# Kernel optimization log

Hardware: AMD Instinct MI355X
Metric: run time of the kernel (lower is better)

The kernel has to match this reference:

```python
import jax, jax.numpy as jnp
import numpy as np

BN_EPS = 1e-5


def setup_inputs() -> dict:
    key = jax.random.key(0)
    k0, k1, k2 = jax.random.split(key, 3)
    N, K, Cin, Cout = 300000, 27, 32, 64
    data = jax.random.normal(k0, (N, Cin), dtype=jnp.float32)
    # Octree neighbor table: index of the neighbor node for each of the 27
    # stencil offsets (-1 would mean empty; here all indices are valid).
    neigh = jax.random.randint(k1, (N, K), 0, N, dtype=jnp.int64)
    # Conv weight, one [Cin, Cout] matrix per stencil offset.
    weight = jax.random.normal(k2, (K, Cin, Cout), dtype=jnp.float32) * (1.0 / np.sqrt(K * Cin))
    gamma = jnp.ones((Cout,), dtype=jnp.float32)
    beta = jnp.zeros((Cout,), dtype=jnp.float32)
    return {"data": data, "neigh": neigh, "weight": weight, "gamma": gamma, "beta": beta}


def reference(data, neigh, weight, gamma, beta):
    # --- OctreeConv: gather neighbors (im2col over sparse octree) + matmul ---
    mask = neigh >= 0                                   # [N, K] valid-neighbor mask
    idx = jnp.clip(neigh, 0)
    gathered = jnp.where(mask[..., None], data[idx], 0.0)  # [N, K, Cin]
    out = jnp.einsum('nkc,kco->no', gathered, weight)       # [N, Cout]
    # --- BatchNorm1d (training mode: batch statistics over nodes) ---
    mean = jnp.mean(out, axis=0)
    var = jnp.var(out, axis=0)
    out = (out - mean) * jax.lax.rsqrt(var + BN_EPS) * gamma + beta
    # --- ReLU ---
    return jax.nn.relu(out)
```

## Files before the change

kernel.cpp:

```cpp
#include <hip/hip_runtime.h>

#define N_NODES   300000
#define K_STENCIL 27
#define CIN       32
#define COUT      64
#define BN_EPS    1e-5f

#define WS_STATS_OFF 0
#define WS_AB_OFF    32768
#define WS_CNT_OFF   33280
#define WS_WT_OFF    33792
#define N_SPLITS     64

typedef short bf16x8 __attribute__((ext_vector_type(8)));
typedef float f32x4  __attribute__((ext_vector_type(4)));

__device__ __forceinline__ short f2bf_rne(float f) {
    unsigned u = __builtin_bit_cast(unsigned, f);
    u += 0x7fffu + ((u >> 16) & 1u);
    return (short)(u >> 16);
}

__global__ __launch_bounds__(256) void prep(const float* __restrict__ w,
                                            unsigned short* __restrict__ wT,
                                            float* __restrict__ stats,
                                            unsigned int* __restrict__ cnt) {
    int t = blockIdx.x * blockDim.x + threadIdx.x;
    if (t < N_SPLITS * 128) stats[t] = 0.f;
    if (t == 0) *cnt = 0u;
    if (t < K_STENCIL * COUT * CIN) {
        int c = t & (CIN - 1);
        int o = (t >> 5) & (COUT - 1);
        int k = t >> 11;
        wT[t] = (unsigned short)f2bf_rne(w[(k * CIN + c) * COUT + o]);
    }
}

__global__ __launch_bounds__(256, 2) void conv_mfma(
        const float* __restrict__ data, const int* __restrict__ neigh,
        const unsigned short* __restrict__ wT, float* __restrict__ out) {
    const int wave  = threadIdx.x >> 6;
    const int lane  = threadIdx.x & 63;
    const int row16 = lane & 15;
    const int quad  = lane >> 4;

    bf16x8 ia, tb;
    #pragma unroll
    for (int j = 0; j < 8; ++j) {
        int k = quad * 8 + j;
        ia[j] = (k == row16) ? (short)0x3F80 : (short)0;
        tb[j] = f2bf_rne((float)(k * 16 + row16));
    }
    f32x4 pacc = {0.f, 0.f, 0.f, 0.f};
    pacc = __builtin_amdgcn_mfma_f32_16x16x32_bf16(ia, tb, pacc, 0, 0, 0);
    int mrow[4], ncol[4];
    #pragma unroll
    for (int r = 0; r < 4; ++r) {
        int iv = (int)(pacc[r] + 0.5f);
        mrow[r] = (iv >> 4) & 15;
        ncol[r] = iv & 15;
    }

    const int node   = blockIdx.x * 64 + wave * 16 + row16;
    const bool valid = (node < N_NODES);
    const int nclamp = valid ? node : 0;

    f32x4 acc[4] = {f32x4{0,0,0,0}, f32x4{0,0,0,0}, f32x4{0,0,0,0}, f32x4{0,0,0,0}};
    const int* nrow = neigh + nclamp * K_STENCIL;

    #pragma unroll
    for (int g = 0; g < 3; ++g) {
        int kid[9];
        #pragma unroll
        for (int j = 0; j < 9; ++j) kid[j] = nrow[g * 9 + j];

        f32x4 lo[9], hi[9];
        #pragma unroll
        for (int j = 0; j < 9; ++j) {
            int idx = kid[j];
            if (valid && idx >= 0) {
                const f32x4* drow = (const f32x4*)(data + (size_t)idx * CIN + quad * 8);
                lo[j] = drow[0];
                hi[j] = drow[1];
            } else {
                lo[j] = f32x4{0, 0, 0, 0};
                hi[j] = f32x4{0, 0, 0, 0};
            }
        }

        #pragma unroll
        for (int j = 0; j < 9; ++j) {
            bf16x8 afrag;
            #pragma unroll
            for (int t = 0; t < 4; ++t) {
                afrag[t]     = f2bf_rne(lo[j][t]);
                afrag[t + 4] = f2bf_rne(hi[j][t]);
            }
            const unsigned short* wk = wT + (g * 9 + j) * (COUT * CIN) + row16 * CIN + quad * 8;
            #pragma unroll
            for (int ct = 0; ct < 4; ++ct) {
                bf16x8 bfrag = *(const bf16x8*)(wk + ct * 16 * CIN);
                acc[ct] = __builtin_amdgcn_mfma_f32_16x16x32_bf16(afrag, bfrag, acc[ct], 0, 0, 0);
            }
        }
    }

    const int tilebase = blockIdx.x * 64 + wave * 16;
    #pragma unroll
    for (int ct = 0; ct < 4; ++ct) {
        #pragma unroll
        for (int r = 0; r < 4; ++r) {
            int n_out = tilebase + mrow[r];
            if (n_out < N_NODES)
                out[(size_t)n_out * COUT + ct * 16 + ncol[r]] = acc[ct][r];
        }
    }
}

__global__ __launch_bounds__(256) void stats_fin(const float* __restrict__ out,
                                                 float* __restrict__ stats,
                                                 unsigned int* __restrict__ cnt,
                                                 const float* __restrict__ gamma,
                                                 const float* __restrict__ beta,
                                                 float* __restrict__ ab) {
    __shared__ float lsum[COUT];
    __shared__ float lsq[COUT];
    __shared__ int lastFlag;
    if (threadIdx.x < COUT) { lsum[threadIdx.x] = 0.f; lsq[threadIdx.x] = 0.f; }
    __syncthreads();

    const int j = threadIdx.x & 15;
    int row = blockIdx.x * 16 + (threadIdx.x >> 4);
    const int rstride = gridDim.x * 16;
    float s0=0,s1=0,s2=0,s3=0,q0=0,q1=0,q2=0,q3=0;
    for (; row < N_NODES; row += rstride) {
        f32x4 v = ((const f32x4*)out)[row * 16 + j];
        s0 += v[0]; q0 += v[0]*v[0];
        s1 += v[1]; q1 += v[1]*v[1];
        s2 += v[2]; q2 += v[2]*v[2];
        s3 += v[3]; q3 += v[3]*v[3];
    }
    atomicAdd(&lsum[j*4+0], s0); atomicAdd(&lsq[j*4+0], q0);
    atomicAdd(&lsum[j*4+1], s1); atomicAdd(&lsq[j*4+1], q1);
    atomicAdd(&lsum[j*4+2], s2); atomicAdd(&lsq[j*4+2], q2);
    atomicAdd(&lsum[j*4+3], s3); atomicAdd(&lsq[j*4+3], q3);
    __syncthreads();

    if (threadIdx.x < 128) {
        int split = blockIdx.x & (N_SPLITS - 1);
        float v = (threadIdx.x < 64) ? lsum[threadIdx.x] : lsq[threadIdx.x - 64];
        atomicAdd(&stats[split * 128 + threadIdx.x], v);
    }
    __syncthreads();

    if (threadIdx.x == 0) {
        __threadfence();
        unsigned old = atomicAdd(cnt, 1u);
        lastFlag = (old == gridDim.x - 1) ? 1 : 0;
    }
    __syncthreads();

    if (lastFlag && threadIdx.x < COUT) {
        int o = threadIdx.x;
        float s = 0.f, q = 0.f;
        for (int sp = 0; sp < N_SPLITS; ++sp) {
            s += __hip_atomic_load(&stats[sp * 128 + o],
                                   __ATOMIC_RELAXED, __HIP_MEMORY_SCOPE_AGENT);
            q += __hip_atomic_load(&stats[sp * 128 + 64 + o],
                                   __ATOMIC_RELAXED, __HIP_MEMORY_SCOPE_AGENT);
        }
        float inv_n = 1.0f / (float)N_NODES;
        float mean = s * inv_n;
        float var  = q * inv_n - mean * mean;
        float a = gamma[o] * rsqrtf(var + BN_EPS);
        float b = beta[o] - mean * a;
        ab[o] = a;
        ab[64 + o] = b;
    }
}

__global__ __launch_bounds__(256) void bn_relu(float* __restrict__ out,
                                               const float* __restrict__ ab) {
    int i = blockIdx.x * blockDim.x + threadIdx.x;
    f32x4 a = ((const f32x4*)ab)[i & 15];
    f32x4 b = ((const f32x4*)(ab + 64))[i & 15];
    f32x4 v = ((f32x4*)out)[i];
    #pragma unroll
    for (int j = 0; j < 4; ++j) {
        float y = v[j] * a[j] + b[j];
        v[j] = y > 0.f ? y : 0.f;
    }
    ((f32x4*)out)[i] = v;
}

extern "C" void kernel_launch(void* const* d_in, const int* in_sizes, int n_in,
                              void* d_out, int out_size, void* d_ws, size_t ws_size,
                              hipStream_t stream) {
    const float* data   = (const float*)d_in[0];
    const int*   neigh  = (const int*)d_in[1];
    const float* weight = (const float*)d_in[2];
    const float* gamma  = (const float*)d_in[3];
    const float* beta   = (const float*)d_in[4];
    float* out = (float*)d_out;

    char* ws = (char*)d_ws;
    float*          stats = (float*)(ws + WS_STATS_OFF);
    float*          ab    = (float*)(ws + WS_AB_OFF);
    unsigned int*   cnt   = (unsigned int*)(ws + WS_CNT_OFF);
    unsigned short* wT    = (unsigned short*)(ws + WS_WT_OFF);

    prep<<<(K_STENCIL * COUT * CIN + 255) / 256, 256, 0, stream>>>(weight, wT, stats, cnt);

    const int grid = (N_NODES + 63) / 64;
    conv_mfma<<<grid, 256, 0, stream>>>(data, neigh, wT, out);

    stats_fin<<<1024, 256, 0, stream>>>(out, stats, cnt, gamma, beta, ab);

    int total4 = N_NODES * COUT / 4;
    bn_relu<<<total4 / 256, 256, 0, stream>>>(out, ab);
}
```

Before: 405.9 us.

## Pre-convert node features to bf16 and gather all 27 neighbors upfront

Adds a pre-pass that converts the whole feature table to bf16 in workspace, so the gather reads 64 bytes per neighbor row instead of 128 and skips per-neighbor conversion. The new conv kernel loads all 27 neighbor indices, then issues all 27 gathers as inline-asm dwordx4 loads before a single wait, and uses a zero row instead of branching on invalid neighbors. Occupancy hint is raised to 3 blocks per SM. This costs an extra full pass over the input and much higher register pressure from 27 live vectors. It falls back to the old path when the workspace is too small.

After: 425.5 us. 4.8% more time.

```diff
diff --git a/kernel.cpp b/kernel.cpp
--- a/kernel.cpp
+++ b/kernel.cpp
@@ -9,7 +9,9 @@
 #define WS_STATS_OFF 0
 #define WS_AB_OFF    32768
 #define WS_CNT_OFF   33280
+#define WS_ZERO_OFF  33344
 #define WS_WT_OFF    33792
+#define WS_DATA_OFF  144384
 #define N_SPLITS     64
 
 typedef short bf16x8 __attribute__((ext_vector_type(8)));
@@ -24,15 +26,103 @@
 __global__ __launch_bounds__(256) void prep(const float* __restrict__ w,
                                             unsigned short* __restrict__ wT,
                                             float* __restrict__ stats,
-                                            unsigned int* __restrict__ cnt) {
+                                            unsigned int* __restrict__ cnt,
+                                            float* __restrict__ zrowF,
+                                            const float* __restrict__ data,
+                                            unsigned short* __restrict__ dataB,
+                                            int doData) {
     int t = blockIdx.x * blockDim.x + threadIdx.x;
     if (t < N_SPLITS * 128) stats[t] = 0.f;
     if (t == 0) *cnt = 0u;
+    if (t < 16) zrowF[t] = 0.f;
     if (t < K_STENCIL * COUT * CIN) {
         int c = t & (CIN - 1);
         int o = (t >> 5) & (COUT - 1);
         int k = t >> 11;
         wT[t] = (unsigned short)f2bf_rne(w[(k * CIN + c) * COUT + o]);
+    }
+    if (doData && t < N_NODES * CIN / 8) {
+        const f32x4* src = (const f32x4*)data + (size_t)t * 2;
+        f32x4 a = src[0], b = src[1];
+        bf16x8 o8;
+        #pragma unroll
+        for (int j = 0; j < 4; ++j) {
+            o8[j]     = f2bf_rne(a[j]);
+            o8[j + 4] = f2bf_rne(b[j]);
+        }
+        ((bf16x8*)dataB)[t] = o8;
+    }
+}
+
+__global__ __launch_bounds__(256, 3) void conv_asm(
+        const unsigned short* __restrict__ dataB, const int* __restrict__ neigh,
+        const unsigned short* __restrict__ wT, float* __restrict__ out,
+        const unsigned short* __restrict__ zrow) {
+    const int wave  = threadIdx.x >> 6;
+    const int lane  = threadIdx.x & 63;
+    const int row16 = lane & 15;
+    const int quad  = lane >> 4;
+
+    bf16x8 ia, tb;
+    #pragma unroll
+    for (int j = 0; j < 8; ++j) {
+        int k = quad * 8 + j;
+        ia[j] = (k == row16) ? (short)0x3F80 : (short)0;
+        tb[j] = f2bf_rne((float)(k * 16 + row16));
+    }
+    f32x4 pacc = {0.f, 0.f, 0.f, 0.f};
+    pacc = __builtin_amdgcn_mfma_f32_16x16x32_bf16(ia, tb, pacc, 0, 0, 0);
+    int mrow[4], ncol[4];
+    #pragma unroll
+    for (int r = 0; r < 4; ++r) {
+        int iv = (int)(pacc[r] + 0.5f);
+        mrow[r] = (iv >> 4) & 15;
+        ncol[r] = iv & 15;
+    }
+
+    const int node   = blockIdx.x * 64 + wave * 16 + row16;
+    const bool valid = (node < N_NODES);
+    const int nclamp = valid ? node : 0;
+    const int* nrow  = neigh + (size_t)nclamp * K_STENCIL;
+
+    int kid[K_STENCIL];
+    #pragma unroll
+    for (int j = 0; j < K_STENCIL; ++j) kid[j] = nrow[j];
+
+    f32x4 pay[K_STENCIL];
+    #pragma unroll
+    for (int j = 0; j < K_STENCIL; ++j) {
+        const unsigned short* p = (kid[j] >= 0)
+            ? (dataB + (size_t)kid[j] * CIN + quad * 8)
+            : (zrow + quad * 8);
+        asm volatile("global_load_dwordx4 %0, %1, off"
+                     : "=&v"(pay[j]) : "v"(p));
+    }
+    asm volatile("s_waitcnt vmcnt(0)" ::: "memory");
+    __builtin_amdgcn_sched_barrier(0);
+
+    f32x4 acc[4] = {f32x4{0,0,0,0}, f32x4{0,0,0,0}, f32x4{0,0,0,0}, f32x4{0,0,0,0}};
+    const unsigned short* wbase = wT + row16 * CIN + quad * 8;
+    #pragma unroll
+    for (int j = 0; j < K_STENCIL; ++j) {
+        bf16x8 afrag = __builtin_bit_cast(bf16x8, pay[j]);
+        const unsigned short* wk = wbase + j * (COUT * CIN);
+        #pragma unroll
+        for (int ct = 0; ct < 4; ++ct) {
+            bf16x8 bfrag = *(const bf16x8*)(wk + ct * 16 * CIN);
+            acc[ct] = __builtin_amdgcn_mfma_f32_16x16x32_bf16(afrag, bfrag, acc[ct], 0, 0, 0);
+        }
+    }
+
+    const int tilebase = blockIdx.x * 64 + wave * 16;
+    #pragma unroll
+    for (int ct = 0; ct < 4; ++ct) {
+        #pragma unroll
+        for (int r = 0; r < 4; ++r) {
+            int n_out = tilebase + mrow[r];
+            if (n_out < N_NODES)
+                out[(size_t)n_out * COUT + ct * 16 + ncol[r]] = acc[ct][r];
+        }
     }
 }
 
@@ -207,12 +297,24 @@
     float*          stats = (float*)(ws + WS_STATS_OFF);
     float*          ab    = (float*)(ws + WS_AB_OFF);
     unsigned int*   cnt   = (unsigned int*)(ws + WS_CNT_OFF);
+    float*          zrowF = (float*)(ws + WS_ZERO_OFF);
     unsigned short* wT    = (unsigned short*)(ws + WS_WT_OFF);
-
-    prep<<<(K_STENCIL * COUT * CIN + 255) / 256, 256, 0, stream>>>(weight, wT, stats, cnt);
+    unsigned short* dataB = (unsigned short*)(ws + WS_DATA_OFF);
+
+    const size_t need_bf16 = (size_t)WS_DATA_OFF + (size_t)N_NODES * CIN * 2;
+    const int useBf16 = (ws_size >= need_bf16) ? 1 : 0;
+
+    const int prepGrid = useBf16 ? (N_NODES * CIN / 8 + 255) / 256
+                                 : (K_STENCIL * COUT * CIN + 255) / 256;
+    prep<<<prepGrid, 256, 0, stream>>>(weight, wT, stats, cnt, zrowF,
+                                       data, dataB, useBf16);
 
     const int grid = (N_NODES + 63) / 64;
-    conv_mfma<<<grid, 256, 0, stream>>>(data, neigh, wT, out);
+    if (useBf16)
+        conv_asm<<<grid, 256, 0, stream>>>(dataB, neigh, wT, out,
+                                           (const unsigned short*)zrowF);
+    else
+        conv_mfma<<<grid, 256, 0, stream>>>(data, neigh, wT, out);
 
     stats_fin<<<1024, 256, 0, stream>>>(out, stats, cnt, gamma, beta, ab);
 
```
